# Optimization experiments

Measured on AMD Instinct MI355X. Metric: run time of the kernel, lower is better.

## Reference

```python
import jax, jax.numpy as jnp
import numpy as np

T, B, NS, NC = 100, 4096, 12, 4
N = NS + NC  # tau dim


def setup_inputs() -> dict:
    key = jax.random.key(0)
    k1, k2, k3, k4, k5 = jax.random.split(key, 5)
    # Symmetric PD quadratic cost C = L L^T / N + I  -> well conditioned
    L = jax.random.normal(k1, (T, B, N, N), dtype=jnp.float32) * 0.1
    C = jnp.einsum('tbij,tbkj->tbik', L, L) + jnp.eye(N, dtype=jnp.float32)
    c = jax.random.normal(k2, (T, B, N), dtype=jnp.float32)
    # Linear dynamics x' = F [x;u] + f, state block near identity for stability
    F = jax.random.normal(k3, (T - 1, B, NS, N), dtype=jnp.float32) * 0.02
    A0 = jnp.concatenate([0.99 * jnp.eye(NS, dtype=jnp.float32),
                          jnp.zeros((NS, NC), jnp.float32)], axis=-1)
    F = F + A0  # broadcast over (T-1, B)
    f = jax.random.normal(k4, (T - 1, B, NS), dtype=jnp.float32) * 0.01
    x_init = jax.random.normal(k5, (B, NS), dtype=jnp.float32)
    return {"x_init": x_init, "C": C, "c": c, "F": F, "f": f}


def _lqr_solve(x_init, C, c, F, f):
    ns = x_init.shape[-1]
    # Pad dynamics to length T (terminal step has no dynamics; V starts at 0
    # so the padded zero F/f contribute nothing).
    Fp = jnp.concatenate([F, jnp.zeros_like(F[:1])], axis=0)  # [T,B,ns,n]
    fp = jnp.concatenate([f, jnp.zeros_like(f[:1])], axis=0)  # [T,B,ns]

    def bwd_step(carry, inp):
        V, v = carry                      # [B,ns,ns], [B,ns]
        Ct, ct, Ft, ft = inp
        # Q = C + F^T V F ; q = c + F^T (V f + v)
        Q = Ct + jnp.einsum('bsi,bst,btj->bij', Ft, V, Ft)
        Vf = jnp.einsum('bst,bt->bs', V, ft) + v
        q = ct + jnp.einsum('bsi,bs->bi', Ft, Vf)
        Qxx, Qxu = Q[:, :ns, :ns], Q[:, :ns, ns:]
        Qux, Quu = Q[:, ns:, :ns], Q[:, ns:, ns:]
        qx, qu = q[:, :ns], q[:, ns:]
        # Joint solve for K = -Quu^{-1} Qux, k = -Quu^{-1} qu
        Kk = -jnp.linalg.solve(Quu, jnp.concatenate([Qux, qu[..., None]], axis=-1))
        K, k = Kk[..., :ns], Kk[..., ns]
        Vn = Qxx + jnp.einsum('bij,bjk->bik', Qxu, K)
        Vn = 0.5 * (Vn + jnp.swapaxes(Vn, -1, -2))
        vn = qx + jnp.einsum('bij,bj->bi', Qxu, k)
        return (Vn, vn), (K, k)

    V0 = jnp.zeros((x_init.shape[0], ns, ns), C.dtype)
    v0 = jnp.zeros((x_init.shape[0], ns), C.dtype)
    _, (Kr, kr) = jax.lax.scan(bwd_step, (V0, v0),
                               (C[::-1], c[::-1], Fp[::-1], fp[::-1]))
    K, k = Kr[::-1], kr[::-1]  # [T,B,nc,ns], [T,B,nc]

    def fwd_step(x, inp):
        Ct, ct, Ft, ft, Kt, kt = inp
        u = jnp.einsum('bij,bj->bi', Kt, x) + kt
        tau = jnp.concatenate([x, u], axis=-1)
        cost = 0.5 * jnp.einsum('bi,bij,bj->b', tau, Ct, tau) \
               + jnp.einsum('bi,bi->b', ct, tau)
        xn = jnp.einsum('bij,bj->bi', Ft, tau) + ft
        return xn, (x, u, cost)

    _, (xs, us, costs) = jax.lax.scan(fwd_step, x_init, (C, c, Fp, fp, K, k))
    return xs, us, jnp.sum(costs, axis=0)


def reference(x_init, C, c, F, f):
    # MPC with QuadCost + LinDx and no box constraints: the iLQR loop
    # converges in one exact LQR solve (Riccati backward + forward rollout).
    x, u, objs = _lqr_solve(x_init, C, c, F, f)
    return x, u, objs
```

## Files before the change

### kernel.cpp

```cpp
#include <hip/hip_runtime.h>
#include <hip/hip_fp16.h>

#define TT 100
#define BB 4096
#define GS 488


#define FENCE() asm volatile("s_waitcnt lgkmcnt(0)" ::: "memory")

__device__ __forceinline__ float quadsum(float x){
  int a = __builtin_amdgcn_update_dpp(0, __float_as_int(x), 0xB1, 0xF, 0xF, true);
  x += __int_as_float(a);
  int c = __builtin_amdgcn_update_dpp(0, __float_as_int(x), 0x4E, 0xF, 0xF, true);
  x += __int_as_float(c);
  return x;
}
__device__ __forceinline__ float readlanef(float x, int srclane){
  return __int_as_float(__builtin_amdgcn_readlane(__float_as_int(x), srclane));
}
template<int CTRL>
__device__ __forceinline__ float ror_add(float x){
  int r = __builtin_amdgcn_update_dpp(0, __float_as_int(x), CTRL, 0xF, 0xF, true);
  return x + __int_as_float(r);
}
__device__ __forceinline__ float reduce16_dpp(float x){
  x = ror_add<0x128>(x); x = ror_add<0x124>(x);
  x = ror_add<0x122>(x); x = ror_add<0x121>(x);
  return x;
}

template<int KMODE>
__device__ __forceinline__ void storeK(void* wsv, size_t of, int l, float X0,float X1,float X2,float X3){
  if (KMODE==0){
    float* wsb=(float*)wsv + of*52;
    if (l<12)       ((float4*)wsb)[l]  = make_float4(X0,X1,X2,X3);
    else if (l==12) ((float4*)wsb)[12] = make_float4(X0,X1,X2,X3);
  } else {
    __half* wsb=(__half*)wsv + of*52;
    if (l<12){
      wsb[l*4+0]=__float2half(X0); wsb[l*4+1]=__float2half(X1);
      wsb[l*4+2]=__float2half(X2); wsb[l*4+3]=__float2half(X3);
    } else if (l==12){
      wsb[48]=__float2half(X0); wsb[49]=__float2half(X1);
      wsb[50]=__float2half(X2); wsb[51]=__float2half(X3);
    }
  }
}
template<int KMODE>
__device__ __forceinline__ float4 loadKcol(const void* wsv, size_t of, int l){
  if (KMODE==0) return ((const float4*)((const float*)wsv + of*52))[l];
  const __half* p=(const __half*)wsv + of*52 + l*4;
  return make_float4(__half2float(p[0]),__half2float(p[1]),__half2float(p[2]),__half2float(p[3]));
}
template<int KMODE>
__device__ __forceinline__ float loadkk(const void* wsv, size_t of, int r){
  if (KMODE==0) return ((const float*)wsv)[of*52+48+r];
  return __half2float(((const __half*)wsv)[of*52+48+r]);
}

template<int KMODE>
__global__ __launch_bounds__(256)
void lqr_fused(const float* __restrict__ xinit,
               const float* __restrict__ Cg,
               const float* __restrict__ cg,
               const float* __restrict__ Fg,
               const float* __restrict__ fg,
               float* __restrict__ out,
               void* __restrict__ wsv)
{
  __shared__ float smem[GS*4];
  const int tid  = threadIdx.x;
  const int lane = tid & 63;
  const int wv   = tid >> 6;
  const int b    = blockIdx.x*4 + wv;
  const int l    = lane >> 2;
  const int qd   = lane & 3;

  float* __restrict__ Vb = smem + wv*GS;
  float* __restrict__ Fl = Vb + 144;
  float* __restrict__ vv = Vb + 384;
  float* __restrict__ tb = Vb + 396;

  if (l<12){
    const int i0=3*qd;
    Vb[l*12+i0]=0.f; Vb[l*12+i0+1]=0.f; Vb[l*12+i0+2]=0.f;
    if (qd==0) vv[l]=0.f;
  }

  float4 sCq; float sc_;
  float4 sFst=make_float4(0,0,0,0); float sftv=0.f;
  {
    const size_t of = ((size_t)(TT-1)*BB + b);
    sCq = ((const float4*)(Cg + of*256 + l*16))[qd];
    sc_ = cg[of*16+l];
  }

  for (int tt=TT-1; tt>=0; --tt){
    const bool hasF = (tt < TT-1);
    const float4 Cq=sCq; const float rc=sc_;
    const float4 Fst=sFst; const float ftv=sftv;

    if (hasF){
      if (lane<48) *(float4*)(Fl + l*20 + 4*qd) = Fst;
      if (qd==0 && l<12) tb[l]=ftv;
    }
    FENCE();

    if (tt>0){
      const size_t of = ((size_t)(tt-1)*BB + b);
      sCq = ((const float4*)(Cg + of*256 + l*16))[qd];
      sc_ = cg[of*16+l];
      if (lane<48) sFst = ((const float4*)(Fg + of*192))[lane];
      if (qd==0 && l<12) sftv = fg[of*12+l];
    }

    float Qf[16];
    {
      const float cx=Cq.x, cy=Cq.y, cz=Cq.z, cw=Cq.w;
      Qf[0] =(qd==0)?cx:0.f; Qf[1] =(qd==0)?cy:0.f; Qf[2] =(qd==0)?cz:0.f; Qf[3] =(qd==0)?cw:0.f;
      Qf[4] =(qd==1)?cx:0.f; Qf[5] =(qd==1)?cy:0.f; Qf[6] =(qd==1)?cz:0.f; Qf[7] =(qd==1)?cw:0.f;
      Qf[8] =(qd==2)?cx:0.f; Qf[9] =(qd==2)?cy:0.f; Qf[10]=(qd==2)?cz:0.f; Qf[11]=(qd==2)?cw:0.f;
      Qf[12]=(qd==3)?cx:0.f; Qf[13]=(qd==3)?cy:0.f; Qf[14]=(qd==3)?cz:0.f; Qf[15]=(qd==3)?cw:0.f;
    }
    float qf=0.f;
    if (hasF){
      float Ftj[12];
      #pragma unroll
      for (int t=0;t<12;t++) Ftj[t]=Fl[t*20+l];
      const int s0=3*qd;
      float W[3];
      #pragma unroll
      for (int j=0;j<3;j++){
        const float4* vr=(const float4*)(Vb+(s0+j)*12);
        float4 v0=vr[0],v1=vr[1],v2=vr[2];
        W[j]= v0.x*Ftj[0]+v0.y*Ftj[1]+v0.z*Ftj[2]+v0.w*Ftj[3]
            + v1.x*Ftj[4]+v1.y*Ftj[5]+v1.z*Ftj[6]+v1.w*Ftj[7]
            + v2.x*Ftj[8]+v2.y*Ftj[9]+v2.z*Ftj[10]+v2.w*Ftj[11];
      }
      #pragma unroll
      for (int j=0;j<3;j++){
        const float4* fr=(const float4*)(Fl+(s0+j)*20);
        float4 f0=fr[0],f1=fr[1],f2=fr[2],f3=fr[3];
        const float w=W[j];
        Qf[0]+=f0.x*w;  Qf[1]+=f0.y*w;  Qf[2]+=f0.z*w;  Qf[3]+=f0.w*w;
        Qf[4]+=f1.x*w;  Qf[5]+=f1.y*w;  Qf[6]+=f1.z*w;  Qf[7]+=f1.w*w;
        Qf[8]+=f2.x*w;  Qf[9]+=f2.y*w;  Qf[10]+=f2.z*w; Qf[11]+=f2.w*w;
        Qf[12]+=f3.x*w; Qf[13]+=f3.y*w; Qf[14]+=f3.z*w; Qf[15]+=f3.w*w;
        qf += w*tb[s0+j];
      }
      const float fta = qd==0?Ftj[0]:qd==1?Ftj[3]:qd==2?Ftj[6]:Ftj[9];
      const float ftb = qd==0?Ftj[1]:qd==1?Ftj[4]:qd==2?Ftj[7]:Ftj[10];
      const float ftc = qd==0?Ftj[2]:qd==1?Ftj[5]:qd==2?Ftj[8]:Ftj[11];
      qf += fta*vv[s0] + ftb*vv[s0+1] + ftc*vv[s0+2];
    }

    #pragma unroll
    for (int i=0;i<16;i++) Qf[i] = quadsum(Qf[i]);
    const float qv = rc + quadsum(qf);

    float a00=readlanef(Qf[12],48),a01=readlanef(Qf[12],52),a02=readlanef(Qf[12],56),a03=readlanef(Qf[12],60);
    float a10=readlanef(Qf[13],48),a11=readlanef(Qf[13],52),a12=readlanef(Qf[13],56),a13=readlanef(Qf[13],60);
    float a20=readlanef(Qf[14],48),a21=readlanef(Qf[14],52),a22=readlanef(Qf[14],56),a23=readlanef(Qf[14],60);
    float a30=readlanef(Qf[15],48),a31=readlanef(Qf[15],52),a32=readlanef(Qf[15],56),a33=readlanef(Qf[15],60);
    const float qu0=readlanef(qv,48),qu1=readlanef(qv,52),qu2=readlanef(qv,56),qu3=readlanef(qv,60);

    float b0=-Qf[12],b1=-Qf[13],b2=-Qf[14],b3=-Qf[15];
    const float i0=1.0f/a00;
    const float m10=a10*i0,m20=a20*i0,m30=a30*i0;
    a11-=m10*a01;a12-=m10*a02;a13-=m10*a03;
    a21-=m20*a01;a22-=m20*a02;a23-=m20*a03;
    a31-=m30*a01;a32-=m30*a02;a33-=m30*a03;
    b1-=m10*b0;b2-=m20*b0;b3-=m30*b0;
    const float i1=1.0f/a11;
    const float m21=a21*i1,m31=a31*i1;
    a22-=m21*a12;a23-=m21*a13;
    a32-=m31*a12;a33-=m31*a13;
    b2-=m21*b1;b3-=m31*b1;
    const float i2=1.0f/a22;
    const float m32=a32*i2;
    a33-=m32*a23;
    b3-=m32*b2;
    const float X3=b3/a33;
    const float X2=(b2-a23*X3)*i2;
    const float X1=(b1-a12*X2-a13*X3)*i1;
    const float X0=(b0-a01*X1-a02*X2-a03*X3)*i0;
    float c0=-qu0,c1=-qu1,c2=-qu2,c3=-qu3;
    c1-=m10*c0;c2-=m20*c0;c3-=m30*c0;
    c2-=m21*c1;c3-=m31*c1;
    c3-=m32*c2;
    const float k3=c3/a33;
    const float k2v=(c2-a23*k3)*i2;
    const float k1=(c1-a12*k2v-a13*k3)*i1;
    const float k0=(c0-a01*k1-a02*k2v-a03*k3)*i0;

    if (qd==0)
      storeK<KMODE>(wsv, (size_t)tt*BB+b, l,
                    l<12?X0:k0, l<12?X1:k1, l<12?X2:k2v, l<12?X3:k3);

    const float base0 = qd==0?Qf[0]:qd==1?Qf[3]:qd==2?Qf[6]:Qf[9];
    const float base1 = qd==0?Qf[1]:qd==1?Qf[4]:qd==2?Qf[7]:Qf[10];
    const float base2 = qd==0?Qf[2]:qd==1?Qf[5]:qd==2?Qf[8]:Qf[11];
    float vn0=base0, vn1=base1, vn2=base2;
    #pragma unroll
    for (int r=0;r<4;r++){
      const float Xr = r==0?X0:r==1?X1:r==2?X2:X3;
      vn0 += __shfl(base0, 48+4*r+qd, 64) * Xr;
      vn1 += __shfl(base1, 48+4*r+qd, 64) * Xr;
      vn2 += __shfl(base2, 48+4*r+qd, 64) * Xr;
    }
    if (l<12){
      const int i0i=3*qd;
      Vb[l*12+i0i]=vn0; Vb[l*12+i0i+1]=vn1; Vb[l*12+i0i+2]=vn2;
      if (qd==0)
        vv[l] = qv + Qf[12]*k0 + Qf[13]*k1 + Qf[14]*k2v + Qf[15]*k3;
    }
  }

  asm volatile("s_waitcnt vmcnt(0)" ::: "memory");

  const int fl = lane & 15;
  const int g4 = lane >> 4;

  float xj = (g4==0 && fl<12)? xinit[(size_t)b*12+fl] : 0.f;
  double costacc=0.0;

  float4 sCa; float sc2_;
  float4 sF0=make_float4(0,0,0,0),sF1=sF0,sF2=sF0,sF3=sF0; float sf_=0.f;
  float4 sK=make_float4(0,0,0,0); float sk_=0.f;
  {
    const float4* pc=(const float4*)(Cg + (size_t)b*256 + fl*16);
    sCa=pc[g4];
    sc2_=cg[(size_t)b*16+fl];
    if (g4==0 && fl<12){
      const float4* pf=(const float4*)(Fg + (size_t)b*192 + fl*16);
      sF0=pf[0];sF1=pf[1];sF2=pf[2];sF3=pf[3];
      sf_=fg[(size_t)b*12+fl];
      sK=loadKcol<KMODE>(wsv,(size_t)b,fl);
    }
    if (g4==0 && fl>=12) sk_=loadkk<KMODE>(wsv,(size_t)b,fl-12);
  }

  for (int t=0;t<TT;t++){
    float4 Ca=sCa; float rc=sc2_;
    float4 F0=sF0,F1=sF1,F2=sF2,F3=sF3; float rf=sf_;
    float4 K4=sK; float kl=sk_;

    if (t+1<TT){
      const size_t of=((size_t)(t+1)*BB + b);
      const float4* pc=(const float4*)(Cg + of*256 + fl*16);
      sCa=pc[g4];
      sc2_=cg[of*16+fl];
      if (g4==0 && fl<12){
        sK=loadKcol<KMODE>(wsv,of,fl);
        if (t+1<TT-1){
          const float4* pf=(const float4*)(Fg + of*192 + fl*16);
          sF0=pf[0];sF1=pf[1];sF2=pf[2];sF3=pf[3];
          sf_=fg[of*12+fl];
        }
      }
      if (g4==0 && fl>=12) sk_=loadkk<KMODE>(wsv,of,fl-12);
    }

    float pr0=0.f,pr1=0.f,pr2=0.f,pr3=0.f;
    if (g4==0 && fl<12){ pr0=K4.x*xj; pr1=K4.y*xj; pr2=K4.z*xj; pr3=K4.w*xj; }
    pr0=reduce16_dpp(pr0); pr1=reduce16_dpp(pr1);
    pr2=reduce16_dpp(pr2); pr3=reduce16_dpp(pr3);

    float* tbuf = tb + (t&1)*16;
    float tauj=0.f;
    if (g4==0){
      if (fl<12) tauj=xj;
      else {
        const float ur=(fl==12)?pr0:(fl==13)?pr1:(fl==14)?pr2:pr3;
        tauj=ur+kl;
      }
      tbuf[fl]=tauj;
    }
    FENCE();

    const float taul = tbuf[fl];
    const float4 tq = ((const float4*)tbuf)[g4];

    const float dot_p = Ca.x*tq.x + Ca.y*tq.y + Ca.z*tq.z + Ca.w*tq.w;
    costacc += (double)( taul*0.5f*dot_p + (g4==0 ? taul*rc : 0.f) );

    if (g4==0){
      if (fl<12) out[(size_t)t*BB*12 + (size_t)b*12 + fl] = xj;
      else       out[(size_t)TT*BB*12 + (size_t)t*BB*4 + (size_t)b*4 + (fl-12)] = tauj;
    }

    if (t<TT-1 && g4==0 && fl<12){
      const float4* tp=(const float4*)tbuf;
      const float4 t0=tp[0],t1=tp[1],t2=tp[2],t3=tp[3];
      xj = rf
         + F0.x*t0.x+F0.y*t0.y+F0.z*t0.z+F0.w*t0.w
         + F1.x*t1.x+F1.y*t1.y+F1.z*t1.z+F1.w*t1.w
         + F2.x*t2.x+F2.y*t2.y+F2.z*t2.z+F2.w*t2.w
         + F3.x*t3.x+F3.y*t3.y+F3.z*t3.z+F3.w*t3.w;
    }
  }

  costacc+=__shfl_xor(costacc,1,64);  costacc+=__shfl_xor(costacc,2,64);
  costacc+=__shfl_xor(costacc,4,64);  costacc+=__shfl_xor(costacc,8,64);
  costacc+=__shfl_xor(costacc,16,64); costacc+=__shfl_xor(costacc,32,64);
  if (lane==0) out[(size_t)TT*BB*16 + b]=(float)costacc;
}

extern "C" void kernel_launch(void* const* d_in, const int* in_sizes, int n_in,
                              void* d_out, int out_size, void* d_ws, size_t ws_size,
                              hipStream_t stream){
  (void)in_sizes; (void)n_in; (void)out_size;
  const float* xinit=(const float*)d_in[0];
  const float* C    =(const float*)d_in[1];
  const float* c    =(const float*)d_in[2];
  const float* F    =(const float*)d_in[3];
  const float* f    =(const float*)d_in[4];
  const size_t need_f32 = (size_t)TT*BB*52*sizeof(float);
  if (ws_size >= need_f32){
    lqr_fused<0><<<dim3(BB/4), dim3(256), 0, stream>>>(xinit,C,c,F,f,(float*)d_out,d_ws);
  } else {
    lqr_fused<1><<<dim3(BB/4), dim3(256), 0, stream>>>(xinit,C,c,F,f,(float*)d_out,d_ws);
  }
}
```

Measured before the change: 463.7 us.

## Give each lane whole Q columns in backward Riccati step to drop quad reductions

```diff
diff --git a/kernel.cpp b/kernel.cpp
--- a/kernel.cpp
+++ b/kernel.cpp
@@ -8,6 +8,10 @@
 
 #define FENCE() asm volatile("s_waitcnt lgkmcnt(0)" ::: "memory")
 
+template<int CTRL>
+__device__ __forceinline__ float qbcast(float x){
+  return __int_as_float(__builtin_amdgcn_update_dpp(0, __float_as_int(x), CTRL, 0xF, 0xF, true));
+}
 __device__ __forceinline__ float quadsum(float x){
   int a = __builtin_amdgcn_update_dpp(0, __float_as_int(x), 0xB1, 0xF, 0xF, true);
   x += __int_as_float(a);
@@ -82,9 +86,8 @@
   float* __restrict__ tb = Vb + 396;
 
   if (l<12){
-    const int i0=3*qd;
-    Vb[l*12+i0]=0.f; Vb[l*12+i0+1]=0.f; Vb[l*12+i0+2]=0.f;
-    if (qd==0) vv[l]=0.f;
+    if (qd<3) *(float4*)(Vb + l*12 + 4*qd) = make_float4(0,0,0,0);
+    else vv[l]=0.f;
   }
 
   float4 sCq; float sc_;
@@ -114,76 +117,79 @@
       if (qd==0 && l<12) sftv = fg[of*12+l];
     }
 
-    float Qf[16];
-    {
-      const float cx=Cq.x, cy=Cq.y, cz=Cq.z, cw=Cq.w;
-      Qf[0] =(qd==0)?cx:0.f; Qf[1] =(qd==0)?cy:0.f; Qf[2] =(qd==0)?cz:0.f; Qf[3] =(qd==0)?cw:0.f;
-      Qf[4] =(qd==1)?cx:0.f; Qf[5] =(qd==1)?cy:0.f; Qf[6] =(qd==1)?cz:0.f; Qf[7] =(qd==1)?cw:0.f;
-      Qf[8] =(qd==2)?cx:0.f; Qf[9] =(qd==2)?cy:0.f; Qf[10]=(qd==2)?cz:0.f; Qf[11]=(qd==2)?cw:0.f;
-      Qf[12]=(qd==3)?cx:0.f; Qf[13]=(qd==3)?cy:0.f; Qf[14]=(qd==3)?cz:0.f; Qf[15]=(qd==3)?cw:0.f;
-    }
+    float Qr0=Cq.x, Qr1=Cq.y, Qr2=Cq.z, Qr3=Cq.w;
     float qf=0.f;
     if (hasF){
       float Ftj[12];
       #pragma unroll
       for (int t=0;t<12;t++) Ftj[t]=Fl[t*20+l];
       const int s0=3*qd;
-      float W[3];
+      float W0,W1,W2;
+      {
+        const float4* vr0=(const float4*)(Vb+(s0+0)*12);
+        const float4* vr1=(const float4*)(Vb+(s0+1)*12);
+        const float4* vr2=(const float4*)(Vb+(s0+2)*12);
+        float4 a0=vr0[0],a1=vr0[1],a2=vr0[2];
+        W0 = a0.x*Ftj[0]+a0.y*Ftj[1]+a0.z*Ftj[2]+a0.w*Ftj[3]
+           + a1.x*Ftj[4]+a1.y*Ftj[5]+a1.z*Ftj[6]+a1.w*Ftj[7]
+           + a2.x*Ftj[8]+a2.y*Ftj[9]+a2.z*Ftj[10]+a2.w*Ftj[11];
+        float4 b0=vr1[0],b1=vr1[1],b2=vr1[2];
+        W1 = b0.x*Ftj[0]+b0.y*Ftj[1]+b0.z*Ftj[2]+b0.w*Ftj[3]
+           + b1.x*Ftj[4]+b1.y*Ftj[5]+b1.z*Ftj[6]+b1.w*Ftj[7]
+           + b2.x*Ftj[8]+b2.y*Ftj[9]+b2.z*Ftj[10]+b2.w*Ftj[11];
+        float4 c0=vr2[0],c1=vr2[1],c2=vr2[2];
+        W2 = c0.x*Ftj[0]+c0.y*Ftj[1]+c0.z*Ftj[2]+c0.w*Ftj[3]
+           + c1.x*Ftj[4]+c1.y*Ftj[5]+c1.z*Ftj[6]+c1.w*Ftj[7]
+           + c2.x*Ftj[8]+c2.y*Ftj[9]+c2.z*Ftj[10]+c2.w*Ftj[11];
+      }
+      float Wf[12];
+      Wf[0] =qbcast<0x00>(W0); Wf[1] =qbcast<0x00>(W1); Wf[2] =qbcast<0x00>(W2);
+      Wf[3] =qbcast<0x55>(W0); Wf[4] =qbcast<0x55>(W1); Wf[5] =qbcast<0x55>(W2);
+      Wf[6] =qbcast<0xAA>(W0); Wf[7] =qbcast<0xAA>(W1); Wf[8] =qbcast<0xAA>(W2);
+      Wf[9] =qbcast<0xFF>(W0); Wf[10]=qbcast<0xFF>(W1); Wf[11]=qbcast<0xFF>(W2);
       #pragma unroll
-      for (int j=0;j<3;j++){
-        const float4* vr=(const float4*)(Vb+(s0+j)*12);
-        float4 v0=vr[0],v1=vr[1],v2=vr[2];
-        W[j]= v0.x*Ftj[0]+v0.y*Ftj[1]+v0.z*Ftj[2]+v0.w*Ftj[3]
-            + v1.x*Ftj[4]+v1.y*Ftj[5]+v1.z*Ftj[6]+v1.w*Ftj[7]
-            + v2.x*Ftj[8]+v2.y*Ftj[9]+v2.z*Ftj[10]+v2.w*Ftj[11];
-      }
-      #pragma unroll
-      for (int j=0;j<3;j++){
-        const float4* fr=(const float4*)(Fl+(s0+j)*20);
-        float4 f0=fr[0],f1=fr[1],f2=fr[2],f3=fr[3];
-        const float w=W[j];
-        Qf[0]+=f0.x*w;  Qf[1]+=f0.y*w;  Qf[2]+=f0.z*w;  Qf[3]+=f0.w*w;
-        Qf[4]+=f1.x*w;  Qf[5]+=f1.y*w;  Qf[6]+=f1.z*w;  Qf[7]+=f1.w*w;
-        Qf[8]+=f2.x*w;  Qf[9]+=f2.y*w;  Qf[10]+=f2.z*w; Qf[11]+=f2.w*w;
-        Qf[12]+=f3.x*w; Qf[13]+=f3.y*w; Qf[14]+=f3.z*w; Qf[15]+=f3.w*w;
-        qf += w*tb[s0+j];
-      }
+      for (int s=0;s<12;s++){
+        const float4 f4 = *(const float4*)(Fl + s*20 + 4*qd);
+        Qr0 += f4.x*Wf[s]; Qr1 += f4.y*Wf[s];
+        Qr2 += f4.z*Wf[s]; Qr3 += f4.w*Wf[s];
+      }
+      qf = W0*tb[s0] + W1*tb[s0+1] + W2*tb[s0+2];
       const float fta = qd==0?Ftj[0]:qd==1?Ftj[3]:qd==2?Ftj[6]:Ftj[9];
       const float ftb = qd==0?Ftj[1]:qd==1?Ftj[4]:qd==2?Ftj[7]:Ftj[10];
       const float ftc = qd==0?Ftj[2]:qd==1?Ftj[5]:qd==2?Ftj[8]:Ftj[11];
       qf += fta*vv[s0] + ftb*vv[s0+1] + ftc*vv[s0+2];
     }
-
-    #pragma unroll
-    for (int i=0;i<16;i++) Qf[i] = quadsum(Qf[i]);
     const float qv = rc + quadsum(qf);
 
-    float a00=readlanef(Qf[12],48),a01=readlanef(Qf[12],52),a02=readlanef(Qf[12],56),a03=readlanef(Qf[12],60);
-    float a10=readlanef(Qf[13],48),a11=readlanef(Qf[13],52),a12=readlanef(Qf[13],56),a13=readlanef(Qf[13],60);
-    float a20=readlanef(Qf[14],48),a21=readlanef(Qf[14],52),a22=readlanef(Qf[14],56),a23=readlanef(Qf[14],60);
-    float a30=readlanef(Qf[15],48),a31=readlanef(Qf[15],52),a32=readlanef(Qf[15],56),a33=readlanef(Qf[15],60);
+    float a00=readlanef(Qr0,51),a01=readlanef(Qr0,55),a02=readlanef(Qr0,59),a03=readlanef(Qr0,63);
+    float a10=readlanef(Qr1,51),a11=readlanef(Qr1,55),a12=readlanef(Qr1,59),a13=readlanef(Qr1,63);
+    float a20=readlanef(Qr2,51),a21=readlanef(Qr2,55),a22=readlanef(Qr2,59),a23=readlanef(Qr2,63);
+    float a30=readlanef(Qr3,51),a31=readlanef(Qr3,55),a32=readlanef(Qr3,59),a33=readlanef(Qr3,63);
     const float qu0=readlanef(qv,48),qu1=readlanef(qv,52),qu2=readlanef(qv,56),qu3=readlanef(qv,60);
 
-    float b0=-Qf[12],b1=-Qf[13],b2=-Qf[14],b3=-Qf[15];
+    const float b0=-qbcast<0xFF>(Qr0), b1=-qbcast<0xFF>(Qr1),
+                b2=-qbcast<0xFF>(Qr2), b3=-qbcast<0xFF>(Qr3);
+    float bb0=b0,bb1=b1,bb2=b2,bb3=b3;
+
     const float i0=1.0f/a00;
     const float m10=a10*i0,m20=a20*i0,m30=a30*i0;
     a11-=m10*a01;a12-=m10*a02;a13-=m10*a03;
     a21-=m20*a01;a22-=m20*a02;a23-=m20*a03;
     a31-=m30*a01;a32-=m30*a02;a33-=m30*a03;
-    b1-=m10*b0;b2-=m20*b0;b3-=m30*b0;
+    bb1-=m10*bb0;bb2-=m20*bb0;bb3-=m30*bb0;
     const float i1=1.0f/a11;
     const float m21=a21*i1,m31=a31*i1;
     a22-=m21*a12;a23-=m21*a13;
     a32-=m31*a12;a33-=m31*a13;
-    b2-=m21*b1;b3-=m31*b1;
+    bb2-=m21*bb1;bb3-=m31*bb1;
     const float i2=1.0f/a22;
     const float m32=a32*i2;
     a33-=m32*a23;
-    b3-=m32*b2;
-    const float X3=b3/a33;
-    const float X2=(b2-a23*X3)*i2;
-    const float X1=(b1-a12*X2-a13*X3)*i1;
-    const float X0=(b0-a01*X1-a02*X2-a03*X3)*i0;
+    bb3-=m32*bb2;
+    const float X3=bb3/a33;
+    const float X2=(bb2-a23*X3)*i2;
+    const float X1=(bb1-a12*X2-a13*X3)*i1;
+    const float X0=(bb0-a01*X1-a02*X2-a03*X3)*i0;
     float c0=-qu0,c1=-qu1,c2=-qu2,c3=-qu3;
     c1-=m10*c0;c2-=m20*c0;c3-=m30*c0;
     c2-=m21*c1;c3-=m31*c1;
@@ -197,22 +203,21 @@
       storeK<KMODE>(wsv, (size_t)tt*BB+b, l,
                     l<12?X0:k0, l<12?X1:k1, l<12?X2:k2v, l<12?X3:k3);
 
-    const float base0 = qd==0?Qf[0]:qd==1?Qf[3]:qd==2?Qf[6]:Qf[9];
-    const float base1 = qd==0?Qf[1]:qd==1?Qf[4]:qd==2?Qf[7]:Qf[10];
-    const float base2 = qd==0?Qf[2]:qd==1?Qf[5]:qd==2?Qf[8]:Qf[11];
-    float vn0=base0, vn1=base1, vn2=base2;
+    float vn0=Qr0, vn1=Qr1, vn2=Qr2, vn3=Qr3;
     #pragma unroll
     for (int r=0;r<4;r++){
       const float Xr = r==0?X0:r==1?X1:r==2?X2:X3;
-      vn0 += __shfl(base0, 48+4*r+qd, 64) * Xr;
-      vn1 += __shfl(base1, 48+4*r+qd, 64) * Xr;
-      vn2 += __shfl(base2, 48+4*r+qd, 64) * Xr;
+      vn0 += __shfl(Qr0, 48+4*r+qd, 64) * Xr;
+      vn1 += __shfl(Qr1, 48+4*r+qd, 64) * Xr;
+      vn2 += __shfl(Qr2, 48+4*r+qd, 64) * Xr;
+      vn3 += __shfl(Qr3, 48+4*r+qd, 64) * Xr;
     }
     if (l<12){
-      const int i0i=3*qd;
-      Vb[l*12+i0i]=vn0; Vb[l*12+i0i+1]=vn1; Vb[l*12+i0i+2]=vn2;
-      if (qd==0)
-        vv[l] = qv + Qf[12]*k0 + Qf[13]*k1 + Qf[14]*k2v + Qf[15]*k3;
+      if (qd<3){
+        *(float4*)(Vb + l*12 + 4*qd) = make_float4(vn0,vn1,vn2,vn3);
+      } else {
+        vv[l] = qv + Qr0*k0 + Qr1*k1 + Qr2*k2v + Qr3*k3;
+      }
     }
   }
 
```

Result: faster. 440.8 us (-4.9%).
